# Kernel optimization log

Measured on AMD Instinct MI355X. Metric: run time of the kernel, lower is better.

Reference implementation:

```python
import jax, jax.numpy as jnp
import numpy as np

W_PULL = 1.0
W_PUSH = 1.0
W_NORM = 0.001
W_EDGE = 10.0
DELTA_V = 0.5
DELTA_D = 1.5
CE_W = 1.0
DICE_W = 1.0
IGN = -100
NUM_CLASSES = 8
EMBED_DIM = 16
NUM_INST = 16  # instance ids 1..16, 0 = background
EPS_C = 1e-8
EPS_D = 1e-5


def setup_inputs() -> dict:
    key = jax.random.key(0)
    k1, k2, k3, k4 = jax.random.split(key, 4)
    B, D, H, W = 2, 64, 128, 128
    return {
        "sem_logits": jax.random.normal(k1, (B, NUM_CLASSES, D, H, W), jnp.float32),
        "instance_embed": jax.random.normal(k2, (B, EMBED_DIM, D, H, W), jnp.float32),
        "class_labels": jax.random.randint(k3, (B, D, H, W), 0, NUM_CLASSES, dtype=jnp.int32),
        "labels": jax.random.randint(k4, (B, D, H, W), 0, NUM_INST + 1, dtype=jnp.int32),
    }


def _ce_loss(logits, target):
    # nn.CrossEntropyLoss(ignore_index=-100), mean over valid voxels
    logp = jax.nn.log_softmax(logits, axis=1)
    valid = (target != IGN)
    t_safe = jnp.where(valid, target, 0)
    nll = -jnp.take_along_axis(logp, t_safe[:, None].astype(jnp.int32), axis=1)[:, 0]
    v = valid.astype(logits.dtype)
    return (nll * v).sum() / jnp.maximum(v.sum(), 1.0)


def _dice_loss(logits, target):
    C = logits.shape[1]
    probs = jax.nn.softmax(logits, axis=1)
    valid = (target != IGN)
    t_safe = jnp.where(valid, target, 0)
    one_hot = jax.nn.one_hot(t_safe, C, dtype=probs.dtype, axis=1)  # [B,C,D,H,W]
    vm = valid[:, None].astype(probs.dtype)
    probs = probs * vm
    one_hot = one_hot * vm
    axes = tuple(range(2, probs.ndim))
    inter = (probs * one_hot).sum(axes)
    card_p = probs.sum(axes)
    card_g = one_hot.sum(axes)
    dice = (2.0 * inter + EPS_D) / (card_p + card_g + EPS_D)
    return 1.0 - dice.mean()


def _boundary_weight(labels):
    # morphological gradient: 3x3x3 max-pool minus min-pool, replicate pad
    lf = labels.astype(jnp.float32)
    p = jnp.pad(lf, ((0, 0), (1, 1), (1, 1), (1, 1)), mode='edge')
    mx = jax.lax.reduce_window(p, -jnp.inf, jax.lax.max, (1, 3, 3, 3), (1, 1, 1, 1), 'VALID')
    mn = jax.lax.reduce_window(p, jnp.inf, jax.lax.min, (1, 3, 3, 3), (1, 1, 1, 1), 'VALID')
    boundary = (mx != mn).astype(jnp.float32)
    return 1.0 + boundary * (W_EDGE - 1.0)


def _instance_loss(embed, labels, w):
    B, C = embed.shape[:2]
    e_flat = embed.reshape(B, C, -1)   # [B,C,N]
    l_flat = labels.reshape(B, -1)     # [B,N]
    w_flat = w.reshape(B, -1)          # [B,N] (w_bone == 1 since weight_bone==1.0)
    K = NUM_INST

    def per_batch(e, l, wv):
        seg = lambda x: jax.ops.segment_sum(x, l, num_segments=K + 1)
        wsum = seg(wv)                       # [K+1]
        cnt = seg(jnp.ones_like(wv))         # [K+1]
        cnum = seg((e * wv).T)               # [K+1, C]
        centers = cnum / (wsum[:, None] + EPS_C)
        cg = centers[l]                      # [N, C] gather own-instance center
        dist = jnp.linalg.norm(e.T - cg, axis=-1)
        pull_sum = seg(jax.nn.relu(dist - DELTA_V) ** 2 * wv)
        present = cnt[1:] > 0                # ids 1..K
        loss_pull = jnp.where(present, pull_sum[1:] / jnp.maximum(cnt[1:], 1.0), 0.0).sum()
        c = centers[1:]                      # [K, C]
        iu, ju = jnp.triu_indices(K, k=1)
        pw = jnp.linalg.norm(c[iu] - c[ju], axis=-1)
        pv = (present[iu] & present[ju]).astype(pw.dtype)
        npres = present.sum().astype(pw.dtype)
        npairs = npres * (npres - 1.0) / 2.0
        push = jax.nn.relu(2.0 * DELTA_D - pw) ** 2 * pv
        loss_push = jnp.where(npairs > 0, push.sum() / jnp.maximum(npairs, 1.0), 0.0)
        cn = jnp.linalg.norm(c, axis=-1)
        loss_norm = jnp.where(npres > 0, (cn * present).sum() / jnp.maximum(npres, 1.0), 0.0)
        return loss_pull, loss_push, loss_norm, (npres > 0).astype(jnp.float32)

    lp, lpu, ln, val = jax.vmap(per_batch)(e_flat, l_flat, w_flat)
    n = jnp.maximum(val.sum(), 1.0)
    return (W_PULL * lp.sum() + W_PUSH * lpu.sum() + W_NORM * ln.sum()) / n


def reference(sem_logits, instance_embed, class_labels, labels):
    loss_ce = _ce_loss(sem_logits, class_labels)
    loss_dice = _dice_loss(sem_logits, class_labels)
    loss_sem = CE_W * loss_ce + DICE_W * loss_dice
    w_edge = _boundary_weight(labels)
    # weight_bone == 1.0 -> w_bone = ones (scipy EDT branch disabled by module guard)
    loss_ins = _instance_loss(instance_embed, labels, w_edge)
    loss = loss_sem + loss_ins
    return loss, loss_sem, loss_ce, loss_dice, loss_ins
```

## Files before the change

kernel.cpp:

```cpp
#include <hip/hip_runtime.h>

#define DHW (64*128*128)
#define MIR 32

#define OFF_CEM   0
#define OFF_SEGM  1568
#define OFF_PULLM 21152
#define OFF_CTR   22240
#define OFF_CNT   22784
#define ACC_FLOATS 22818
#define BND_BYTE_OFF (128*1024)

typedef __bf16 bf16x8 __attribute__((ext_vector_type(8)));
typedef float f32x4 __attribute__((ext_vector_type(4)));
union FragU { short s[8]; bf16x8 v; };

__device__ inline short f2bf(float f) {
    union { float f; unsigned u; } v; v.f = f;
    unsigned r = v.u + 0x7FFF + ((v.u >> 16) & 1);
    return (short)(r >> 16);
}

__global__ void zero_kernel(float* acc) {
    int i = blockIdx.x * 1024 + threadIdx.x;
    if (i < ACC_FLOATS) acc[i] = 0.0f;
}

__global__ __launch_bounds__(256) void ce_dice_kernel(const float* __restrict__ logits,
                                                      const int* __restrict__ cls,
                                                      float* __restrict__ acc) {
    int b = blockIdx.y;
    int tid = threadIdx.x;
    int vb = (blockIdx.x * 256 + tid) * 4;
    const float* lg = logits + (size_t)b * 8 * DHW;
    const int* cl = cls + (size_t)b * DHW;

    float4 xc[8];
#pragma unroll
    for (int c = 0; c < 8; ++c)
        xc[c] = *reinterpret_cast<const float4*>(&lg[(size_t)c * DHW + vb]);
    int4 t4 = *reinterpret_cast<const int4*>(&cl[vb]);
    int tt[4] = {t4.x, t4.y, t4.z, t4.w};

    float nll = 0.f, cardp[8], inter[8], cardg[8];
#pragma unroll
    for (int c = 0; c < 8; ++c) { cardp[c] = 0.f; inter[c] = 0.f; cardg[c] = 0.f; }

#pragma unroll
    for (int j = 0; j < 4; ++j) {
        float x[8];
#pragma unroll
        for (int c = 0; c < 8; ++c) x[c] = ((const float*)&xc[c])[j];
        int t = tt[j];
        bool valid = (t != -100);
        float mx = x[0];
#pragma unroll
        for (int c = 1; c < 8; ++c) mx = fmaxf(mx, x[c]);
        float e[8], s = 0.f;
#pragma unroll
        for (int c = 0; c < 8; ++c) { e[c] = __expf(x[c] - mx); s += e[c]; }
        float inv = 1.0f / s;
        float lse = __logf(s);
        if (valid) {
#pragma unroll
            for (int c = 0; c < 8; ++c) {
                float p = e[c] * inv;
                cardp[c] += p;
                if (t == c) { inter[c] += p; cardg[c] += 1.f; nll += mx + lse - x[c]; }
            }
        }
    }

    __shared__ float sh[25];
    if (tid < 25) sh[tid] = 0.f;
    __syncthreads();
    int lane = tid & 63;
    float vals[25];
    vals[0] = nll;
#pragma unroll
    for (int c = 0; c < 8; ++c) { vals[1 + c] = cardp[c]; vals[9 + c] = inter[c]; vals[17 + c] = cardg[c]; }
#pragma unroll
    for (int i = 0; i < 25; ++i) {
        float r = vals[i];
#pragma unroll
        for (int off = 32; off > 0; off >>= 1) r += __shfl_down(r, off, 64);
        if (lane == 0) atomicAdd(&sh[i], r);
    }
    __syncthreads();
    if (tid < 25) {
        int mir = blockIdx.x & (MIR - 1);
        int dst;
        if (tid == 0) dst = 0;
        else if (tid < 9) dst = 1 + b * 8 + (tid - 1);
        else if (tid < 17) dst = 17 + b * 8 + (tid - 9);
        else dst = 33 + b * 8 + (tid - 17);
        atomicAdd(&acc[OFF_CEM + mir * 49 + dst], sh[tid]);
    }
}

__global__ __launch_bounds__(256) void boundary_kernel(const int* __restrict__ labels,
                                                       unsigned char* __restrict__ bnd) {
    int b = blockIdx.y;
    int vb = (blockIdx.x * 256 + threadIdx.x) * 4;
    const int* L = labels + (size_t)b * DHW;
    int x = vb & 127, y = (vb >> 7) & 127, z = vb >> 14;
    int4 c = *reinterpret_cast<const int4*>(&L[vb]);
    int z0 = max(z - 1, 0), z1 = min(z + 1, 63);
    int y0 = max(y - 1, 0), y1 = min(y + 1, 127);
    int xm = max(x - 1, 0), xp = min(x + 4, 127);
    unsigned b0 = 0, b1 = 0, b2 = 0, b3 = 0;
    for (int zz = z0; zz <= z1; ++zz) {
        for (int yy = y0; yy <= y1; ++yy) {
            const int* row = L + (zz << 14) + (yy << 7);
            int4 r = *reinterpret_cast<const int4*>(&row[x]);
            int rm = row[xm], rp = row[xp];
            b0 |= (rm != c.x) | (r.x != c.x) | (r.y != c.x);
            b1 |= (r.x != c.y) | (r.y != c.y) | (r.z != c.y);
            b2 |= (r.y != c.z) | (r.z != c.z) | (r.w != c.z);
            b3 |= (r.z != c.w) | (r.w != c.w) | (rp != c.w);
            if (b0 & b1 & b2 & b3) goto done;
        }
    }
done:
    unsigned pack = b0 | (b1 << 8) | (b2 << 16) | (b3 << 24);
    *reinterpret_cast<unsigned*>(&bnd[(size_t)b * DHW + vb]) = pack;
}

__global__ __launch_bounds__(256) void segsum_kernel(const float* __restrict__ embed,
                                                     const int* __restrict__ labels,
                                                     const unsigned char* __restrict__ bnd,
                                                     float* __restrict__ acc) {
    int b = blockIdx.y;
    int tid = threadIdx.x;
    int lane = tid & 63;
    int wv = tid >> 6;
    int m = lane & 15;
    int quad = lane >> 4;

    const int* L = labels + (size_t)b * DHW;
    const float* E = embed + (size_t)b * 16 * DHW + (size_t)m * DHW;
    const unsigned char* Bd = bnd + (size_t)b * DHW;

    int waveId = blockIdx.x * 4 + wv;
    int off = waveId * 256 + quad * 8;

    f32x4 acc_c = {0.f, 0.f, 0.f, 0.f};
    f32x4 acc_w = {0.f, 0.f, 0.f, 0.f};
    f32x4 acc_n = {0.f, 0.f, 0.f, 0.f};

    FragU ones_col;
#pragma unroll
    for (int j = 0; j < 8; ++j) ones_col.s[j] = (m == 0) ? (short)0x3F80 : (short)0;

    int4 l0 = *reinterpret_cast<const int4*>(&L[off]);
    int4 l1 = *reinterpret_cast<const int4*>(&L[off + 4]);
    unsigned bb0 = *reinterpret_cast<const unsigned*>(&Bd[off]);
    unsigned bb1 = *reinterpret_cast<const unsigned*>(&Bd[off + 4]);
    float4 f0 = *reinterpret_cast<const float4*>(&E[off]);
    float4 f1 = *reinterpret_cast<const float4*>(&E[off + 4]);

    for (int i = 0; i < 8; ++i) {
        int4 nl0, nl1; unsigned nb0, nb1; float4 nf0, nf1;
        if (i < 7) {
            int noff = off + 32;
            nl0 = *reinterpret_cast<const int4*>(&L[noff]);
            nl1 = *reinterpret_cast<const int4*>(&L[noff + 4]);
            nb0 = *reinterpret_cast<const unsigned*>(&Bd[noff]);
            nb1 = *reinterpret_cast<const unsigned*>(&Bd[noff + 4]);
            nf0 = *reinterpret_cast<const float4*>(&E[noff]);
            nf1 = *reinterpret_cast<const float4*>(&E[noff + 4]);
        }

        int ls[8] = {l0.x, l0.y, l0.z, l0.w, l1.x, l1.y, l1.z, l1.w};
        float fs[8] = {f0.x, f0.y, f0.z, f0.w, f1.x, f1.y, f1.z, f1.w};

        FragU a, a2, bf;
#pragma unroll
        for (int j = 0; j < 8; ++j) {
            unsigned byte = ((j < 4 ? bb0 : bb1) >> ((j & 3) * 8)) & 0xFF;
            short w = byte ? (short)0x4120 : (short)0x3F80;
            bool hit = (ls[j] == m + 1);
            a.s[j]  = hit ? w : (short)0;
            a2.s[j] = hit ? (short)0x3F80 : (short)0;
            bf.s[j] = f2bf(fs[j]);
        }
        acc_c = __builtin_amdgcn_mfma_f32_16x16x32_bf16(a.v, bf.v, acc_c, 0, 0, 0);
        acc_w = __builtin_amdgcn_mfma_f32_16x16x32_bf16(a.v, ones_col.v, acc_w, 0, 0, 0);
        acc_n = __builtin_amdgcn_mfma_f32_16x16x32_bf16(a2.v, ones_col.v, acc_n, 0, 0, 0);

        l0 = nl0; l1 = nl1; bb0 = nb0; bb1 = nb1; f0 = nf0; f1 = nf1;
        off += 32;
    }

    __shared__ float cacc[288];
    for (int i = tid; i < 288; i += 256) cacc[i] = 0.f;
    __syncthreads();
#pragma unroll
    for (int r = 0; r < 4; ++r)
        atomicAdd(&cacc[(quad * 4 + r) * 16 + m], acc_c[r]);
    if (m == 0) {
#pragma unroll
        for (int r = 0; r < 4; ++r) {
            atomicAdd(&cacc[256 + quad * 4 + r], acc_w[r]);
            atomicAdd(&cacc[272 + quad * 4 + r], acc_n[r]);
        }
    }
    __syncthreads();
    {
        int mir = blockIdx.x & (MIR - 1);
        float* segbase = acc + OFF_SEGM + mir * 612 + b * 306;
        atomicAdd(&segbase[16 + tid], cacc[tid]);
        if (tid < 16) atomicAdd(&segbase[272 + 1 + tid], cacc[256 + tid]);
        else if (tid < 32) atomicAdd(&segbase[289 + 1 + (tid - 16)], cacc[256 + tid]);
    }
}

__global__ __launch_bounds__(1024) void centers_kernel(float* acc) {
    int tid = threadIdx.x;
    if (tid < 544) {
        int b = tid / 272, r = tid % 272;
        int k = r >> 4;
        float cn = 0.f, ws = 0.f;
        for (int mv = 0; mv < MIR; ++mv) {
            const float* segbase = acc + OFF_SEGM + mv * 612 + b * 306;
            if (r >= 16) cn += segbase[r];
            ws += segbase[272 + k];
        }
        acc[OFF_CTR + tid] = (r >= 16) ? cn / (ws + 1e-8f) : 0.f;
    } else if (tid < 578) {
        int j = tid - 544;
        int b = j / 17, k = j % 17;
        float s = 0.f;
        for (int mv = 0; mv < MIR; ++mv)
            s += acc[OFF_SEGM + mv * 612 + b * 306 + 289 + k];
        acc[OFF_CNT + j] = s;
    }
}

__global__ __launch_bounds__(256) void pull_kernel(const float* __restrict__ embed,
                                                   const int* __restrict__ labels,
                                                   const unsigned char* __restrict__ bnd,
                                                   float* __restrict__ acc) {
    int b = blockIdx.y;
    int tid = threadIdx.x;
    int wv = tid >> 6;
    __shared__ float ctr[17 * 16];
    __shared__ float ps[4 * 20];
    for (int i = tid; i < 272; i += 256) ctr[i] = acc[OFF_CTR + b * 272 + i];
    for (int i = tid; i < 80; i += 256) ps[i] = 0.f;
    __syncthreads();

    const int* L = labels + (size_t)b * DHW;
    const float* E = embed + (size_t)b * 16 * DHW;
    const unsigned char* Bd = bnd + (size_t)b * DHW;
    int vb = (blockIdx.x * 256 + tid) * 4;

    int4 l4 = *reinterpret_cast<const int4*>(&L[vb]);
    int l[4] = {l4.x, l4.y, l4.z, l4.w};
    unsigned bb = *reinterpret_cast<const unsigned*>(&Bd[vb]);

    float4 e4[16];
#pragma unroll
    for (int c = 0; c < 16; ++c)
        e4[c] = *reinterpret_cast<const float4*>(&E[(size_t)c * DHW + vb]);

#pragma unroll
    for (int j = 0; j < 4; ++j) {
        if (l[j] != 0) {
            float w = ((bb >> (8 * j)) & 0xFF) ? 10.f : 1.f;
            const float4* cg = reinterpret_cast<const float4*>(&ctr[l[j] * 16]);
            float d2 = 0.f;
#pragma unroll
            for (int q = 0; q < 4; ++q) {
                float4 cv = cg[q];
                float d0 = ((const float*)&e4[4 * q + 0])[j] - cv.x;
                float d1 = ((const float*)&e4[4 * q + 1])[j] - cv.y;
                float dd2 = ((const float*)&e4[4 * q + 2])[j] - cv.z;
                float d3 = ((const float*)&e4[4 * q + 3])[j] - cv.w;
                d2 += d0 * d0 + d1 * d1 + dd2 * dd2 + d3 * d3;
            }
            float d = fmaxf(sqrtf(d2) - 0.5f, 0.f);
            atomicAdd(&ps[wv * 20 + l[j]], d * d * w);
        }
    }
    __syncthreads();
    if (tid >= 1 && tid < 17) {
        float v = ps[tid] + ps[20 + tid] + ps[40 + tid] + ps[60 + tid];
        int mir = blockIdx.x & (MIR - 1);
        if (v != 0.f) atomicAdd(&acc[OFF_PULLM + mir * 34 + b * 17 + tid], v);
    }
}

__global__ __launch_bounds__(256) void finalize_kernel(const float* __restrict__ acc, float* __restrict__ out) {
    __shared__ float s_ce[49], s_pl[34];
    __shared__ float sh_push[2], sh_norm[2], sh_pull[2], sh_npres[2];
    int tid = threadIdx.x;
    if (tid < 49) {
        float s = 0.f;
        for (int mv = 0; mv < MIR; ++mv) s += acc[OFF_CEM + mv * 49 + tid];
        s_ce[tid] = s;
    }
    if (tid >= 64 && tid < 98) {
        int j = tid - 64;
        float s = 0.f;
        for (int mv = 0; mv < MIR; ++mv) s += acc[OFF_PULLM + mv * 34 + j];
        s_pl[j] = s;
    }
    if (tid < 2) { sh_push[tid] = 0.f; sh_norm[tid] = 0.f; sh_pull[tid] = 0.f; sh_npres[tid] = 0.f; }
    __syncthreads();

    if (tid < 32) {
        int b = tid >> 4, k = (tid & 15) + 1;
        float cnt = acc[OFF_CNT + b * 17 + k];
        if (cnt > 0.f) {
            atomicAdd(&sh_npres[b], 1.f);
            atomicAdd(&sh_pull[b], s_pl[b * 17 + k] / fmaxf(cnt, 1.f));
            const float* c = &acc[OFF_CTR + (b * 17 + k) * 16];
            float n2 = 0.f;
            for (int i = 0; i < 16; ++i) n2 += c[i] * c[i];
            atomicAdd(&sh_norm[b], sqrtf(n2));
        }
    }
    for (int t = tid; t < 240; t += blockDim.x) {
        int b = t / 120, p = t % 120;
        int i = 1, rem = p;
        while (rem >= (16 - i)) { rem -= (16 - i); ++i; }
        int j = i + 1 + rem;
        bool pi = acc[OFF_CNT + b * 17 + i] > 0.f;
        bool pj = acc[OFF_CNT + b * 17 + j] > 0.f;
        if (pi && pj) {
            const float* ci = &acc[OFF_CTR + (b * 17 + i) * 16];
            const float* cj = &acc[OFF_CTR + (b * 17 + j) * 16];
            float d2 = 0.f;
            for (int c = 0; c < 16; ++c) { float dd = ci[c] - cj[c]; d2 += dd * dd; }
            float r = fmaxf(3.0f - sqrtf(d2), 0.f);
            atomicAdd(&sh_push[b], r * r);
        }
    }
    __syncthreads();
    if (tid == 0) {
        float nll = s_ce[0];
        float vcnt = 0.f;
        for (int i = 0; i < 16; ++i) vcnt += s_ce[33 + i];
        float ce = nll / fmaxf(vcnt, 1.f);
        float dsum = 0.f;
        for (int i = 0; i < 16; ++i) {
            float it = s_ce[17 + i], cp = s_ce[1 + i], cg = s_ce[33 + i];
            dsum += (2.f * it + 1e-5f) / (cp + cg + 1e-5f);
        }
        float dice = 1.f - dsum / 16.f;
        float lp = 0.f, lpu = 0.f, ln = 0.f, val = 0.f;
        for (int b = 0; b < 2; ++b) {
            float npres = sh_npres[b];
            lp += sh_pull[b];
            float npairs = npres * (npres - 1.f) * 0.5f;
            lpu += (npairs > 0.f) ? sh_push[b] / fmaxf(npairs, 1.f) : 0.f;
            ln += (npres > 0.f) ? sh_norm[b] / fmaxf(npres, 1.f) : 0.f;
            val += (npres > 0.f) ? 1.f : 0.f;
        }
        float n = fmaxf(val, 1.f);
        float ins = (1.0f * lp + 1.0f * lpu + 0.001f * ln) / n;
        float sem = ce + dice;
        out[0] = sem + ins;
        out[1] = sem;
        out[2] = ce;
        out[3] = dice;
        out[4] = ins;
    }
}

extern "C" void kernel_launch(void* const* d_in, const int* in_sizes, int n_in,
                              void* d_out, int out_size, void* d_ws, size_t ws_size,
                              hipStream_t stream) {
    const float* sem = (const float*)d_in[0];
    const float* emb = (const float*)d_in[1];
    const int* cls = (const int*)d_in[2];
    const int* lab = (const int*)d_in[3];
    float* out = (float*)d_out;
    float* acc = (float*)d_ws;
    unsigned char* bnd = (unsigned char*)d_ws + BND_BYTE_OFF;

    hipLaunchKernelGGL(zero_kernel, dim3(23), dim3(1024), 0, stream, acc);
    hipLaunchKernelGGL(ce_dice_kernel, dim3(1024, 2), dim3(256), 0, stream, sem, cls, acc);
    hipLaunchKernelGGL(boundary_kernel, dim3(1024, 2), dim3(256), 0, stream, lab, bnd);
    hipLaunchKernelGGL(segsum_kernel, dim3(1024, 2), dim3(256), 0, stream, emb, lab, bnd, acc);
    hipLaunchKernelGGL(centers_kernel, dim3(1), dim3(1024), 0, stream, acc);
    hipLaunchKernelGGL(pull_kernel, dim3(1024, 2), dim3(256), 0, stream, emb, lab, bnd, acc);
    hipLaunchKernelGGL(finalize_kernel, dim3(1), dim3(256), 0, stream, acc, out);
}
```

Measured before the change: 335.8 us.

## Fuse CE/dice and segment-sum into one kernel; recompute boundary mask inline

Merges the CE/dice kernel and segment-sum kernel into a single front kernel whose blocks alternate roles, so the two independent streams run concurrently in one launch. The boundary kernel and its byte mask buffer are removed. Both the segment-sum and pull passes now recompute the 3x3x3 edge test from the labels as they go. This drops a launch and a write-then-read round trip of the boundary mask, but adds neighbourhood label reads (mostly cache hits) and compute to the two embedding passes, with the stencil done twice.

```diff
diff --git a/kernel.cpp b/kernel.cpp
--- a/kernel.cpp
+++ b/kernel.cpp
@@ -9,7 +9,6 @@
 #define OFF_CTR   22240
 #define OFF_CNT   22784
 #define ACC_FLOATS 22818
-#define BND_BYTE_OFF (128*1024)
 
 typedef __bf16 bf16x8 __attribute__((ext_vector_type(8)));
 typedef float f32x4 __attribute__((ext_vector_type(4)));
@@ -21,90 +20,8 @@
     return (short)(r >> 16);
 }
 
-__global__ void zero_kernel(float* acc) {
-    int i = blockIdx.x * 1024 + threadIdx.x;
-    if (i < ACC_FLOATS) acc[i] = 0.0f;
-}
-
-__global__ __launch_bounds__(256) void ce_dice_kernel(const float* __restrict__ logits,
-                                                      const int* __restrict__ cls,
-                                                      float* __restrict__ acc) {
-    int b = blockIdx.y;
-    int tid = threadIdx.x;
-    int vb = (blockIdx.x * 256 + tid) * 4;
-    const float* lg = logits + (size_t)b * 8 * DHW;
-    const int* cl = cls + (size_t)b * DHW;
-
-    float4 xc[8];
-#pragma unroll
-    for (int c = 0; c < 8; ++c)
-        xc[c] = *reinterpret_cast<const float4*>(&lg[(size_t)c * DHW + vb]);
-    int4 t4 = *reinterpret_cast<const int4*>(&cl[vb]);
-    int tt[4] = {t4.x, t4.y, t4.z, t4.w};
-
-    float nll = 0.f, cardp[8], inter[8], cardg[8];
-#pragma unroll
-    for (int c = 0; c < 8; ++c) { cardp[c] = 0.f; inter[c] = 0.f; cardg[c] = 0.f; }
-
-#pragma unroll
-    for (int j = 0; j < 4; ++j) {
-        float x[8];
-#pragma unroll
-        for (int c = 0; c < 8; ++c) x[c] = ((const float*)&xc[c])[j];
-        int t = tt[j];
-        bool valid = (t != -100);
-        float mx = x[0];
-#pragma unroll
-        for (int c = 1; c < 8; ++c) mx = fmaxf(mx, x[c]);
-        float e[8], s = 0.f;
-#pragma unroll
-        for (int c = 0; c < 8; ++c) { e[c] = __expf(x[c] - mx); s += e[c]; }
-        float inv = 1.0f / s;
-        float lse = __logf(s);
-        if (valid) {
-#pragma unroll
-            for (int c = 0; c < 8; ++c) {
-                float p = e[c] * inv;
-                cardp[c] += p;
-                if (t == c) { inter[c] += p; cardg[c] += 1.f; nll += mx + lse - x[c]; }
-            }
-        }
-    }
-
-    __shared__ float sh[25];
-    if (tid < 25) sh[tid] = 0.f;
-    __syncthreads();
-    int lane = tid & 63;
-    float vals[25];
-    vals[0] = nll;
-#pragma unroll
-    for (int c = 0; c < 8; ++c) { vals[1 + c] = cardp[c]; vals[9 + c] = inter[c]; vals[17 + c] = cardg[c]; }
-#pragma unroll
-    for (int i = 0; i < 25; ++i) {
-        float r = vals[i];
-#pragma unroll
-        for (int off = 32; off > 0; off >>= 1) r += __shfl_down(r, off, 64);
-        if (lane == 0) atomicAdd(&sh[i], r);
-    }
-    __syncthreads();
-    if (tid < 25) {
-        int mir = blockIdx.x & (MIR - 1);
-        int dst;
-        if (tid == 0) dst = 0;
-        else if (tid < 9) dst = 1 + b * 8 + (tid - 1);
-        else if (tid < 17) dst = 17 + b * 8 + (tid - 9);
-        else dst = 33 + b * 8 + (tid - 17);
-        atomicAdd(&acc[OFF_CEM + mir * 49 + dst], sh[tid]);
-    }
-}
-
-__global__ __launch_bounds__(256) void boundary_kernel(const int* __restrict__ labels,
-                                                       unsigned char* __restrict__ bnd) {
-    int b = blockIdx.y;
-    int vb = (blockIdx.x * 256 + threadIdx.x) * 4;
-    const int* L = labels + (size_t)b * DHW;
+__device__ inline unsigned edge4(const int* __restrict__ L, int vb, int4 c) {
     int x = vb & 127, y = (vb >> 7) & 127, z = vb >> 14;
-    int4 c = *reinterpret_cast<const int4*>(&L[vb]);
     int z0 = max(z - 1, 0), z1 = min(z + 1, 63);
     int y0 = max(y - 1, 0), y1 = min(y + 1, 127);
     int xm = max(x - 1, 0), xp = min(x + 4, 127);
@@ -118,100 +35,170 @@
             b1 |= (r.x != c.y) | (r.y != c.y) | (r.z != c.y);
             b2 |= (r.y != c.z) | (r.z != c.z) | (r.w != c.z);
             b3 |= (r.z != c.w) | (r.w != c.w) | (rp != c.w);
-            if (b0 & b1 & b2 & b3) goto done;
-        }
-    }
-done:
-    unsigned pack = b0 | (b1 << 8) | (b2 << 16) | (b3 << 24);
-    *reinterpret_cast<unsigned*>(&bnd[(size_t)b * DHW + vb]) = pack;
-}
-
-__global__ __launch_bounds__(256) void segsum_kernel(const float* __restrict__ embed,
-                                                     const int* __restrict__ labels,
-                                                     const unsigned char* __restrict__ bnd,
-                                                     float* __restrict__ acc) {
-    int b = blockIdx.y;
+            if (b0 & b1 & b2 & b3) return 0xF;
+        }
+    }
+    return b0 | (b1 << 1) | (b2 << 2) | (b3 << 3);
+}
+
+__global__ void zero_kernel(float* acc) {
+    int i = blockIdx.x * 1024 + threadIdx.x;
+    if (i < ACC_FLOATS) acc[i] = 0.0f;
+}
+
+__global__ __launch_bounds__(256) void front_kernel(const float* __restrict__ logits,
+                                                    const float* __restrict__ embed,
+                                                    const int* __restrict__ cls,
+                                                    const int* __restrict__ labels,
+                                                    float* __restrict__ acc) {
+    __shared__ float sh[25];
+    __shared__ float cacc[288];
+    int role = blockIdx.x & 1;
+    int pos = blockIdx.x >> 1;
+    int b = pos & 1;
+    int blk = pos >> 1;
+    int mir = blk & (MIR - 1);
     int tid = threadIdx.x;
-    int lane = tid & 63;
-    int wv = tid >> 6;
-    int m = lane & 15;
-    int quad = lane >> 4;
-
-    const int* L = labels + (size_t)b * DHW;
-    const float* E = embed + (size_t)b * 16 * DHW + (size_t)m * DHW;
-    const unsigned char* Bd = bnd + (size_t)b * DHW;
-
-    int waveId = blockIdx.x * 4 + wv;
-    int off = waveId * 256 + quad * 8;
-
-    f32x4 acc_c = {0.f, 0.f, 0.f, 0.f};
-    f32x4 acc_w = {0.f, 0.f, 0.f, 0.f};
-    f32x4 acc_n = {0.f, 0.f, 0.f, 0.f};
-
-    FragU ones_col;
-#pragma unroll
-    for (int j = 0; j < 8; ++j) ones_col.s[j] = (m == 0) ? (short)0x3F80 : (short)0;
-
-    int4 l0 = *reinterpret_cast<const int4*>(&L[off]);
-    int4 l1 = *reinterpret_cast<const int4*>(&L[off + 4]);
-    unsigned bb0 = *reinterpret_cast<const unsigned*>(&Bd[off]);
-    unsigned bb1 = *reinterpret_cast<const unsigned*>(&Bd[off + 4]);
-    float4 f0 = *reinterpret_cast<const float4*>(&E[off]);
-    float4 f1 = *reinterpret_cast<const float4*>(&E[off + 4]);
-
-    for (int i = 0; i < 8; ++i) {
-        int4 nl0, nl1; unsigned nb0, nb1; float4 nf0, nf1;
-        if (i < 7) {
-            int noff = off + 32;
-            nl0 = *reinterpret_cast<const int4*>(&L[noff]);
-            nl1 = *reinterpret_cast<const int4*>(&L[noff + 4]);
-            nb0 = *reinterpret_cast<const unsigned*>(&Bd[noff]);
-            nb1 = *reinterpret_cast<const unsigned*>(&Bd[noff + 4]);
-            nf0 = *reinterpret_cast<const float4*>(&E[noff]);
-            nf1 = *reinterpret_cast<const float4*>(&E[noff + 4]);
-        }
-
-        int ls[8] = {l0.x, l0.y, l0.z, l0.w, l1.x, l1.y, l1.z, l1.w};
-        float fs[8] = {f0.x, f0.y, f0.z, f0.w, f1.x, f1.y, f1.z, f1.w};
-
-        FragU a, a2, bf;
-#pragma unroll
-        for (int j = 0; j < 8; ++j) {
-            unsigned byte = ((j < 4 ? bb0 : bb1) >> ((j & 3) * 8)) & 0xFF;
-            short w = byte ? (short)0x4120 : (short)0x3F80;
-            bool hit = (ls[j] == m + 1);
-            a.s[j]  = hit ? w : (short)0;
-            a2.s[j] = hit ? (short)0x3F80 : (short)0;
-            bf.s[j] = f2bf(fs[j]);
-        }
-        acc_c = __builtin_amdgcn_mfma_f32_16x16x32_bf16(a.v, bf.v, acc_c, 0, 0, 0);
-        acc_w = __builtin_amdgcn_mfma_f32_16x16x32_bf16(a.v, ones_col.v, acc_w, 0, 0, 0);
-        acc_n = __builtin_amdgcn_mfma_f32_16x16x32_bf16(a2.v, ones_col.v, acc_n, 0, 0, 0);
-
-        l0 = nl0; l1 = nl1; bb0 = nb0; bb1 = nb1; f0 = nf0; f1 = nf1;
-        off += 32;
-    }
-
-    __shared__ float cacc[288];
-    for (int i = tid; i < 288; i += 256) cacc[i] = 0.f;
-    __syncthreads();
-#pragma unroll
-    for (int r = 0; r < 4; ++r)
-        atomicAdd(&cacc[(quad * 4 + r) * 16 + m], acc_c[r]);
-    if (m == 0) {
-#pragma unroll
-        for (int r = 0; r < 4; ++r) {
-            atomicAdd(&cacc[256 + quad * 4 + r], acc_w[r]);
-            atomicAdd(&cacc[272 + quad * 4 + r], acc_n[r]);
-        }
-    }
-    __syncthreads();
-    {
-        int mir = blockIdx.x & (MIR - 1);
-        float* segbase = acc + OFF_SEGM + mir * 612 + b * 306;
-        atomicAdd(&segbase[16 + tid], cacc[tid]);
-        if (tid < 16) atomicAdd(&segbase[272 + 1 + tid], cacc[256 + tid]);
-        else if (tid < 32) atomicAdd(&segbase[289 + 1 + (tid - 16)], cacc[256 + tid]);
+
+    if (role == 0) {
+        int vb = (blk * 256 + tid) * 4;
+        const float* lg = logits + (size_t)b * 8 * DHW;
+        const int* cl = cls + (size_t)b * DHW;
+
+        float4 xc[8];
+#pragma unroll
+        for (int c = 0; c < 8; ++c)
+            xc[c] = *reinterpret_cast<const float4*>(&lg[(size_t)c * DHW + vb]);
+        int4 t4 = *reinterpret_cast<const int4*>(&cl[vb]);
+        int tt[4] = {t4.x, t4.y, t4.z, t4.w};
+
+        float nll = 0.f, cardp[8], inter[8], cardg[8];
+#pragma unroll
+        for (int c = 0; c < 8; ++c) { cardp[c] = 0.f; inter[c] = 0.f; cardg[c] = 0.f; }
+
+#pragma unroll
+        for (int j = 0; j < 4; ++j) {
+            float x[8];
+#pragma unroll
+            for (int c = 0; c < 8; ++c) x[c] = ((const float*)&xc[c])[j];
+            int t = tt[j];
+            bool valid = (t != -100);
+            float mx = x[0];
+#pragma unroll
+            for (int c = 1; c < 8; ++c) mx = fmaxf(mx, x[c]);
+            float e[8], s = 0.f;
+#pragma unroll
+            for (int c = 0; c < 8; ++c) { e[c] = __expf(x[c] - mx); s += e[c]; }
+            float inv = 1.0f / s;
+            float lse = __logf(s);
+            if (valid) {
+#pragma unroll
+                for (int c = 0; c < 8; ++c) {
+                    float p = e[c] * inv;
+                    cardp[c] += p;
+                    if (t == c) { inter[c] += p; cardg[c] += 1.f; nll += mx + lse - x[c]; }
+                }
+            }
+        }
+
+        if (tid < 25) sh[tid] = 0.f;
+        __syncthreads();
+        int lane = tid & 63;
+        float vals[25];
+        vals[0] = nll;
+#pragma unroll
+        for (int c = 0; c < 8; ++c) { vals[1 + c] = cardp[c]; vals[9 + c] = inter[c]; vals[17 + c] = cardg[c]; }
+#pragma unroll
+        for (int i = 0; i < 25; ++i) {
+            float r = vals[i];
+#pragma unroll
+            for (int off = 32; off > 0; off >>= 1) r += __shfl_down(r, off, 64);
+            if (lane == 0) atomicAdd(&sh[i], r);
+        }
+        __syncthreads();
+        if (tid < 25) {
+            int dst;
+            if (tid == 0) dst = 0;
+            else if (tid < 9) dst = 1 + b * 8 + (tid - 1);
+            else if (tid < 17) dst = 17 + b * 8 + (tid - 9);
+            else dst = 33 + b * 8 + (tid - 17);
+            atomicAdd(&acc[OFF_CEM + mir * 49 + dst], sh[tid]);
+        }
+    } else {
+        int lane = tid & 63;
+        int wv = tid >> 6;
+        int m = lane & 15;
+        int quad = lane >> 4;
+
+        const int* L = labels + (size_t)b * DHW;
+        const float* E = embed + (size_t)b * 16 * DHW + (size_t)m * DHW;
+
+        int waveId = blk * 4 + wv;
+        int off = waveId * 256 + quad * 8;
+
+        f32x4 acc_c = {0.f, 0.f, 0.f, 0.f};
+        f32x4 acc_w = {0.f, 0.f, 0.f, 0.f};
+        f32x4 acc_n = {0.f, 0.f, 0.f, 0.f};
+
+        FragU ones_col;
+#pragma unroll
+        for (int j = 0; j < 8; ++j) ones_col.s[j] = (m == 0) ? (short)0x3F80 : (short)0;
+
+        int4 l0 = *reinterpret_cast<const int4*>(&L[off]);
+        int4 l1 = *reinterpret_cast<const int4*>(&L[off + 4]);
+        float4 f0 = *reinterpret_cast<const float4*>(&E[off]);
+        float4 f1 = *reinterpret_cast<const float4*>(&E[off + 4]);
+
+        for (int i = 0; i < 8; ++i) {
+            int4 nl0, nl1; float4 nf0, nf1;
+            if (i < 7) {
+                int noff = off + 32;
+                nl0 = *reinterpret_cast<const int4*>(&L[noff]);
+                nl1 = *reinterpret_cast<const int4*>(&L[noff + 4]);
+                nf0 = *reinterpret_cast<const float4*>(&E[noff]);
+                nf1 = *reinterpret_cast<const float4*>(&E[noff + 4]);
+            }
+            unsigned eb = edge4(L, off, l0) | (edge4(L, off + 4, l1) << 4);
+
+            int ls[8] = {l0.x, l0.y, l0.z, l0.w, l1.x, l1.y, l1.z, l1.w};
+            float fs[8] = {f0.x, f0.y, f0.z, f0.w, f1.x, f1.y, f1.z, f1.w};
+
+            FragU a, a2, bf;
+#pragma unroll
+            for (int j = 0; j < 8; ++j) {
+                short w = ((eb >> j) & 1) ? (short)0x4120 : (short)0x3F80;
+                bool hit = (ls[j] == m + 1);
+                a.s[j]  = hit ? w : (short)0;
+                a2.s[j] = hit ? (short)0x3F80 : (short)0;
+                bf.s[j] = f2bf(fs[j]);
+            }
+            acc_c = __builtin_amdgcn_mfma_f32_16x16x32_bf16(a.v, bf.v, acc_c, 0, 0, 0);
+            acc_w = __builtin_amdgcn_mfma_f32_16x16x32_bf16(a.v, ones_col.v, acc_w, 0, 0, 0);
+            acc_n = __builtin_amdgcn_mfma_f32_16x16x32_bf16(a2.v, ones_col.v, acc_n, 0, 0, 0);
+
+            l0 = nl0; l1 = nl1; f0 = nf0; f1 = nf1;
+            off += 32;
+        }
+
+        for (int i = tid; i < 288; i += 256) cacc[i] = 0.f;
+        __syncthreads();
+#pragma unroll
+        for (int r = 0; r < 4; ++r)
+            atomicAdd(&cacc[(quad * 4 + r) * 16 + m], acc_c[r]);
+        if (m == 0) {
+#pragma unroll
+            for (int r = 0; r < 4; ++r) {
+                atomicAdd(&cacc[256 + quad * 4 + r], acc_w[r]);
+                atomicAdd(&cacc[272 + quad * 4 + r], acc_n[r]);
+            }
+        }
+        __syncthreads();
+        {
+            float* segbase = acc + OFF_SEGM + mir * 612 + b * 306;
+            atomicAdd(&segbase[16 + tid], cacc[tid]);
+            if (tid < 16) atomicAdd(&segbase[272 + 1 + tid], cacc[256 + tid]);
+            else if (tid < 32) atomicAdd(&segbase[289 + 1 + (tid - 16)], cacc[256 + tid]);
+        }
     }
 }
 
@@ -239,9 +226,9 @@
 
 __global__ __launch_bounds__(256) void pull_kernel(const float* __restrict__ embed,
                                                    const int* __restrict__ labels,
-                                                   const unsigned char* __restrict__ bnd,
                                                    float* __restrict__ acc) {
-    int b = blockIdx.y;
+    int b = blockIdx.x & 1;
+    int blk = blockIdx.x >> 1;
     int tid = threadIdx.x;
     int wv = tid >> 6;
     __shared__ float ctr[17 * 16];
@@ -252,22 +239,22 @@
 
     const int* L = labels + (size_t)b * DHW;
     const float* E = embed + (size_t)b * 16 * DHW;
-    const unsigned char* Bd = bnd + (size_t)b * DHW;
-    int vb = (blockIdx.x * 256 + tid) * 4;
+    int vb = (blk * 256 + tid) * 4;
 
     int4 l4 = *reinterpret_cast<const int4*>(&L[vb]);
     int l[4] = {l4.x, l4.y, l4.z, l4.w};
-    unsigned bb = *reinterpret_cast<const unsigned*>(&Bd[vb]);
 
     float4 e4[16];
 #pragma unroll
     for (int c = 0; c < 16; ++c)
         e4[c] = *reinterpret_cast<const float4*>(&E[(size_t)c * DHW + vb]);
 
+    unsigned eb = edge4(L, vb, l4);
+
 #pragma unroll
     for (int j = 0; j < 4; ++j) {
         if (l[j] != 0) {
-            float w = ((bb >> (8 * j)) & 0xFF) ? 10.f : 1.f;
+            float w = ((eb >> j) & 1) ? 10.f : 1.f;
             const float4* cg = reinterpret_cast<const float4*>(&ctr[l[j] * 16]);
             float d2 = 0.f;
 #pragma unroll
@@ -286,7 +273,7 @@
     __syncthreads();
     if (tid >= 1 && tid < 17) {
         float v = ps[tid] + ps[20 + tid] + ps[40 + tid] + ps[60 + tid];
-        int mir = blockIdx.x & (MIR - 1);
+        int mir = blk & (MIR - 1);
         if (v != 0.f) atomicAdd(&acc[OFF_PULLM + mir * 34 + b * 17 + tid], v);
     }
 }
@@ -378,13 +365,10 @@
     const int* lab = (const int*)d_in[3];
     float* out = (float*)d_out;
     float* acc = (float*)d_ws;
-    unsigned char* bnd = (unsigned char*)d_ws + BND_BYTE_OFF;
 
     hipLaunchKernelGGL(zero_kernel, dim3(23), dim3(1024), 0, stream, acc);
-    hipLaunchKernelGGL(ce_dice_kernel, dim3(1024, 2), dim3(256), 0, stream, sem, cls, acc);
-    hipLaunchKernelGGL(boundary_kernel, dim3(1024, 2), dim3(256), 0, stream, lab, bnd);
-    hipLaunchKernelGGL(segsum_kernel, dim3(1024, 2), dim3(256), 0, stream, emb, lab, bnd, acc);
+    hipLaunchKernelGGL(front_kernel, dim3(4096), dim3(256), 0, stream, sem, emb, cls, lab, acc);
     hipLaunchKernelGGL(centers_kernel, dim3(1), dim3(1024), 0, stream, acc);
-    hipLaunchKernelGGL(pull_kernel, dim3(1024, 2), dim3(256), 0, stream, emb, lab, bnd, acc);
+    hipLaunchKernelGGL(pull_kernel, dim3(2048), dim3(256), 0, stream, emb, lab, acc);
     hipLaunchKernelGGL(finalize_kernel, dim3(1), dim3(256), 0, stream, acc, out);
 }
```

Result: slower. 354.1 us (+5.4%).
